# Optimization experiments

Hardware: AMD Instinct MI355X
Metric: run time of the kernel (lower is better)

The kernel has to match this reference:

```python
import jax, jax.numpy as jnp
import numpy as np

NP_, NA, NPR = 3000, 25, 1071
N = NP_ + NA + NPR          # 4096 total nodes
D = 256                     # latent_dim
H = 8                       # num_heads
DH = D // H                 # head dim 32
FF = 4 * D                  # feed-forward dim
BLOCKS = 3                  # args.block_num
E = 131072                  # edges = N * 32 avg degree
EPS = 1e-5


def setup_inputs() -> dict:
    key = jax.random.key(0)
    ks = jax.random.split(key, 16)
    s = 1.0 / np.sqrt(D)
    return {
        "adj_row": jax.random.randint(ks[0], (E,), 0, N, dtype=jnp.int32),
        "adj_col": jax.random.randint(ks[1], (E,), 0, N, dtype=jnp.int32),
        "adj_val": jax.random.uniform(ks[2], (E,), dtype=jnp.float32),
        "pe": jax.random.normal(ks[3], (NP_, D), dtype=jnp.float32) * s,
        "ae": jax.random.normal(ks[4], (NA, D), dtype=jnp.float32) * s,
        "qe": jax.random.normal(ks[5], (NPR, D), dtype=jnp.float32) * s,
        "Wqkv": jax.random.normal(ks[6], (D, 3 * D), dtype=jnp.float32) * s,
        "Wo": jax.random.normal(ks[7], (D, D), dtype=jnp.float32) * s,
        "W1": jax.random.normal(ks[8], (D, FF), dtype=jnp.float32) * s,
        "b1": jnp.zeros((FF,), dtype=jnp.float32),
        "W2": jax.random.normal(ks[9], (FF, D), dtype=jnp.float32) * (1.0 / np.sqrt(FF)),
        "b2": jnp.zeros((D,), dtype=jnp.float32),
        "ln1_g": jnp.ones((D,), dtype=jnp.float32),
        "ln1_b": jnp.zeros((D,), dtype=jnp.float32),
        "ln2_g": jnp.ones((D,), dtype=jnp.float32),
        "ln2_b": jnp.zeros((D,), dtype=jnp.float32),
    }


def _layer_norm(x, g, b):
    m = jnp.mean(x, axis=-1, keepdims=True)
    v = jnp.mean(jnp.square(x - m), axis=-1, keepdims=True)
    return (x - m) * jax.lax.rsqrt(v + EPS) * g + b


def _encoder_layer(x, Wqkv, Wo, W1, b1, W2, b2, ln1_g, ln1_b, ln2_g, ln2_b):
    # x: [N, D]; standard post-LN transformer encoder (dropout = 0)
    qkv = x @ Wqkv                                   # [N, 3D]
    q, k, v = jnp.split(qkv, 3, axis=-1)
    q = q.reshape(N, H, DH)
    k = k.reshape(N, H, DH)
    v = v.reshape(N, H, DH)
    scores = jnp.einsum("nhd,mhd->hnm", q, k) / np.sqrt(DH)  # [H, N, N]
    att = jax.nn.softmax(scores, axis=-1)
    o = jnp.einsum("hnm,mhd->nhd", att, v).reshape(N, D) @ Wo
    x = _layer_norm(x + o, ln1_g, ln1_b)
    h = jax.nn.relu(x @ W1 + b1) @ W2 + b2
    return _layer_norm(x + h, ln2_g, ln2_b)


def _spmm(adj_row, adj_col, adj_val, x):
    # sparse [N,N] @ dense [N,D] via gather + segment-sum scatter
    msgs = adj_val[:, None] * x[adj_col]             # [E, D]
    return jax.ops.segment_sum(msgs, adj_row, num_segments=N)


def reference(adj_row, adj_col, adj_val, pe, ae, qe, Wqkv, Wo, W1, b1, W2, b2,
              ln1_g, ln1_b, ln2_g, ln2_b):
    cur = jnp.concatenate([pe, ae, qe], axis=0)      # [N, D]
    total = cur
    for _ in range(BLOCKS):
        t = _spmm(adj_row, adj_col, adj_val, cur)
        t = _encoder_layer(t, Wqkv, Wo, W1, b1, W2, b2, ln1_g, ln1_b, ln2_g, ln2_b)
        cur = t + cur                                # residual per block
        total = total + cur                          # sum over embeds list
    protein = total[:NP_]
    aa = total[NP_:NP_ + NA]
    prop = total[NP_ + NA:]
    return total, protein, aa, prop
```

## Files before the change

kernel.cpp:

```cpp
#include <hip/hip_runtime.h>
#include <hip/hip_bf16.h>


#define NPROT 3000
#define NAA   25
#define NPROP 1071
#define NTOT  4096
#define DIM   256
#define NH    8
#define DHD   32
#define FFD   1024
#define NEDGE 131072
#define LNEPS 1e-5f
#define KSPLIT 4
#define KVQ (NTOT/KSPLIT)

typedef unsigned short u16;
typedef __attribute__((ext_vector_type(8))) short short8v;
typedef __attribute__((ext_vector_type(4))) float float4v;
typedef __attribute__((ext_vector_type(2))) unsigned int uint2v;

__device__ __forceinline__ u16 f2bu(float x){
  union { __hip_bfloat16 h; u16 u; } c; c.h = __float2bfloat16(x); return c.u;
}
__device__ __forceinline__ float bu2f(u16 u){
  union { unsigned int i; float f; } c; c.i = ((unsigned int)u) << 16; return c.f;
}
__device__ __forceinline__ float4v mfma16(short8v a, short8v b, float4v c){
  return __builtin_amdgcn_mfma_f32_16x16x32_bf16(a, b, c, 0, 0, 0);
}

__global__ __launch_bounds__(256) void k_embed(const float* __restrict__ pe, const float* __restrict__ ae,
                                               const float* __restrict__ qe,
                                               float* __restrict__ cur, float* __restrict__ tot){
  int i = blockIdx.x*256 + threadIdx.x;
  int row = i >> 8;
  float v;
  if (row < NPROT)           v = pe[i];
  else if (row < NPROT+NAA)  v = ae[i - NPROT*DIM];
  else                       v = qe[i - (NPROT+NAA)*DIM];
  cur[i] = v; tot[i] = v;
}

__global__ __launch_bounds__(256) void k_zero(int* __restrict__ p, int n){
  int i = blockIdx.x*256 + threadIdx.x; if (i < n) p[i] = 0;
}

__global__ __launch_bounds__(256) void k_wconv(const float* __restrict__ W, u16* __restrict__ Wt,
                                               int K, int N){
  int n = blockIdx.x;
  for (int k = threadIdx.x; k < K; k += 256)
    Wt[(size_t)n*K + k] = f2bu(W[(size_t)k*N + n]);
}

__global__ __launch_bounds__(256) void k_hist(const int* __restrict__ rows, int* __restrict__ cnt){
  int e = blockIdx.x*256 + threadIdx.x; if (e < NEDGE) atomicAdd(&cnt[rows[e]], 1);
}

__global__ __launch_bounds__(64) void k_scan(const int* __restrict__ cnt, int* __restrict__ rowptr,
                                             int* __restrict__ cursor){
  int lane = threadIdx.x;
  int sum = 0;
  for (int i = 0; i < 64; ++i) sum += cnt[lane*64 + i];
  int pref = sum;
  #pragma unroll
  for (int off = 1; off < 64; off <<= 1){
    int u = __shfl_up(pref, off);
    if (lane >= off) pref += u;
  }
  int run = pref - sum;
  for (int i = 0; i < 64; ++i){
    int c = cnt[lane*64 + i];
    rowptr[lane*64 + i] = run;
    cursor[lane*64 + i] = run;
    run += c;
  }
  if (lane == 63) rowptr[NTOT] = run;
}

__global__ __launch_bounds__(256) void k_scatter(const int* __restrict__ rows, const int* __restrict__ cols,
                                                 const float* __restrict__ vals, int* __restrict__ cursor,
                                                 int* __restrict__ ccol, float* __restrict__ cval){
  int e = blockIdx.x*256 + threadIdx.x; if (e >= NEDGE) return;
  int p = atomicAdd(&cursor[rows[e]], 1);
  ccol[p] = cols[e]; cval[p] = vals[e];
}

__global__ __launch_bounds__(256) void k_spmm(const int* __restrict__ rowptr, const int* __restrict__ ccol,
                                              const float* __restrict__ cval, const float* __restrict__ x,
                                              float* __restrict__ out, u16* __restrict__ outb){
  int r = blockIdx.x, c = threadIdx.x;
  int s = rowptr[r], e = rowptr[r+1];
  float acc = 0.f;
  for (int i = s; i < e; ++i)
    acc += cval[i] * x[((size_t)ccol[i] << 8) + c];
  out[((size_t)r << 8) + c] = acc;
  outb[((size_t)r << 8) + c] = f2bu(acc);
}

template<int RELU, int BIAS, int BF16OUT>
__global__ __launch_bounds__(256) void k_gemm_mfma(const u16* __restrict__ A, const u16* __restrict__ Wt,
                                                   const float* __restrict__ bias, void* __restrict__ Cv,
                                                   int M, int K, int Nc){
  __shared__ u16 Al[128*64];
  __shared__ u16 Bl[128*64];
  const int tid = threadIdx.x;
  const int w  = tid >> 6, l = tid & 63, lr = l & 15, g = l >> 4;
  const int row0 = blockIdx.y*128, col0 = blockIdx.x*128;
  const int wm = (w >> 1)*64, wn = (w & 1)*64;
  const int sm = tid >> 1;
  const int so = (tid & 1)*4;
  float4v acc[4][4] = {};

  for (int k0 = 0; k0 < K; k0 += 64){
    const u16* As = A  + (size_t)(row0 + sm)*K + k0 + so*8;
    const u16* Bs = Wt + (size_t)(col0 + sm)*K + k0 + so*8;
    #pragma unroll
    for (int j = 0; j < 4; ++j){
      int o = so + j;
      int slot = o ^ (sm & 7);
      *(short8v*)(Al + sm*64 + slot*8) = *(const short8v*)(As + j*8);
      *(short8v*)(Bl + sm*64 + slot*8) = *(const short8v*)(Bs + j*8);
    }
    __syncthreads();
    #pragma unroll
    for (int kk = 0; kk < 2; ++kk){
      short8v af[4], bfr[4];
      #pragma unroll
      for (int i = 0; i < 4; ++i){
        int am = wm + 16*i + lr;
        af[i]  = *(const short8v*)(Al + am*64 + (((4*kk + g) ^ (am & 7))*8));
        int bn = wn + 16*i + lr;
        bfr[i] = *(const short8v*)(Bl + bn*64 + (((4*kk + g) ^ (bn & 7))*8));
      }
      #pragma unroll
      for (int mi = 0; mi < 4; ++mi)
        #pragma unroll
        for (int ni = 0; ni < 4; ++ni)
          acc[mi][ni] = mfma16(af[mi], bfr[ni], acc[mi][ni]);
    }
    __syncthreads();
  }

  #pragma unroll
  for (int mi = 0; mi < 4; ++mi){
    #pragma unroll
    for (int ni = 0; ni < 4; ++ni){
      int col = col0 + wn + 16*ni + lr;
      float bv = BIAS ? bias[col] : 0.f;
      #pragma unroll
      for (int j = 0; j < 4; ++j){
        int row = row0 + wm + 16*mi + 4*g + j;
        float v = acc[mi][ni][j] + bv;
        if (RELU) v = fmaxf(v, 0.f);
        if (BF16OUT) ((u16*)Cv)[(size_t)row*Nc + col] = f2bu(v);
        else         ((float*)Cv)[(size_t)row*Nc + col] = v;
      }
    }
  }
}

__global__ __launch_bounds__(256) void k_attn_mfma(const u16* __restrict__ qbf,
                                                   u16* __restrict__ op,
                                                   float* __restrict__ mbuf, float* __restrict__ lbuf){
  __shared__ u16 Vt[2][32*64];
  __shared__ u16 Pl[4][16*64];
  __shared__ float Fl[4][16];
  const int h   = blockIdx.y;
  const int ks  = blockIdx.z;
  const int qb  = blockIdx.x * 64;
  const int tid = threadIdx.x;
  const int w   = tid >> 6;
  const int l   = tid & 63;
  const int lr  = l & 15;
  const int g   = l >> 4;
  const int sr  = tid >> 2;
  const int sq  = tid & 3;
  const float SC  = 0.17677669529663687f;
  const float SCL = 0.25503837f;
  u16* opart = op + (size_t)ks*NTOT*DIM;

  short8v qf = *(const short8v*)(qbf + (size_t)(qb + 16*w + lr)*768 + h*DHD + 8*g);

  float4v oa0 = {0.f,0.f,0.f,0.f}, oa1 = {0.f,0.f,0.f,0.f};
  float mrun = -1e30f, lrun = 0.f;
  u16* pw = &Pl[w][0];

  const u16* vp = qbf + (size_t)(ks*KVQ + sr)*768 + 512 + h*DHD + 8*sq;
  const u16* kp = qbf + (size_t)(ks*KVQ + lr)*768 + 256 + h*DHD + 8*g;
  short8v vreg = *(const short8v*)vp;
  short8v kf0 = *(const short8v*)(kp);
  short8v kf1 = *(const short8v*)(kp + (size_t)16*768);
  short8v kf2 = *(const short8v*)(kp + (size_t)32*768);
  short8v kf3 = *(const short8v*)(kp + (size_t)48*768);

  const int NIT = KVQ/64;
  for (int t = 0; t < NIT; ++t){
    u16* vt = &Vt[t & 1][0];
    #pragma unroll
    for (int j = 0; j < 8; ++j){
      int row  = 8*sq + j;
      int slot = (sr >> 3) ^ j;
      vt[row*64 + slot*8 + (sr & 7)] = (u16)vreg[j];
    }
    __syncthreads();
    vp += (size_t)64*768;
    if (t + 1 < NIT) vreg = *(const short8v*)vp;

    float4v s0 = mfma16(kf0, qf, (float4v){0.f,0.f,0.f,0.f});
    float4v s1 = mfma16(kf1, qf, (float4v){0.f,0.f,0.f,0.f});
    float4v s2 = mfma16(kf2, qf, (float4v){0.f,0.f,0.f,0.f});
    float4v s3 = mfma16(kf3, qf, (float4v){0.f,0.f,0.f,0.f});
    if (t + 1 < NIT){
      const u16* kn = kp + (size_t)(t+1)*64*768;
      kf0 = *(const short8v*)(kn);
      kf1 = *(const short8v*)(kn + (size_t)16*768);
      kf2 = *(const short8v*)(kn + (size_t)32*768);
      kf3 = *(const short8v*)(kn + (size_t)48*768);
    }

    float tm = fmaxf(fmaxf(fmaxf(s0[0],s0[1]),fmaxf(s0[2],s0[3])),
              fmaxf(fmaxf(fmaxf(s1[0],s1[1]),fmaxf(s1[2],s1[3])),
              fmaxf(fmaxf(fmaxf(s2[0],s2[1]),fmaxf(s2[2],s2[3])),
                    fmaxf(fmaxf(s3[0],s3[1]),fmaxf(s3[2],s3[3])))));
    tm = fmaxf(tm, __shfl_xor(tm, 16));
    tm = fmaxf(tm, __shfl_xor(tm, 32));
    float mn  = fmaxf(mrun, tm);
    float fac = exp2f((mrun - mn)*SCL);
    float mns = mn*SCL;
    mrun = mn;
    float rs = 0.f;
    #pragma unroll
    for (int j = 0; j < 4; ++j){
      float p0 = exp2f(__builtin_fmaf(s0[j], SCL, -mns)); s0[j] = p0;
      float p1 = exp2f(__builtin_fmaf(s1[j], SCL, -mns)); s1[j] = p1;
      float p2 = exp2f(__builtin_fmaf(s2[j], SCL, -mns)); s2[j] = p2;
      float p3 = exp2f(__builtin_fmaf(s3[j], SCL, -mns)); s3[j] = p3;
      rs += (p0 + p1) + (p2 + p3);
    }
    rs += __shfl_xor(rs, 16);
    rs += __shfl_xor(rs, 32);
    lrun = lrun*fac + rs;
    if (g == 0) Fl[w][lr] = fac;

    {
      unsigned int a0 = (unsigned)f2bu(s0[0]) | ((unsigned)f2bu(s0[1]) << 16);
      unsigned int b0 = (unsigned)f2bu(s0[2]) | ((unsigned)f2bu(s0[3]) << 16);
      unsigned int a1 = (unsigned)f2bu(s1[0]) | ((unsigned)f2bu(s1[1]) << 16);
      unsigned int b1 = (unsigned)f2bu(s1[2]) | ((unsigned)f2bu(s1[3]) << 16);
      unsigned int a2 = (unsigned)f2bu(s2[0]) | ((unsigned)f2bu(s2[1]) << 16);
      unsigned int b2 = (unsigned)f2bu(s2[2]) | ((unsigned)f2bu(s2[3]) << 16);
      unsigned int a3 = (unsigned)f2bu(s3[0]) | ((unsigned)f2bu(s3[1]) << 16);
      unsigned int b3 = (unsigned)f2bu(s3[2]) | ((unsigned)f2bu(s3[3]) << 16);
      int gh = g >> 1, gl = 4*(g & 1);
      uint2v* d0 = (uint2v*)(pw + lr*64 + ((0 + gh) ^ (lr & 7))*8 + gl);
      uint2v* d1 = (uint2v*)(pw + lr*64 + ((2 + gh) ^ (lr & 7))*8 + gl);
      uint2v* d2 = (uint2v*)(pw + lr*64 + ((4 + gh) ^ (lr & 7))*8 + gl);
      uint2v* d3 = (uint2v*)(pw + lr*64 + ((6 + gh) ^ (lr & 7))*8 + gl);
      *d0 = (uint2v){a0, b0};
      *d1 = (uint2v){a1, b1};
      *d2 = (uint2v){a2, b2};
      *d3 = (uint2v){a3, b3};
    }

    float fq0 = Fl[w][4*g+0], fq1 = Fl[w][4*g+1], fq2 = Fl[w][4*g+2], fq3 = Fl[w][4*g+3];
    oa0[0]*=fq0; oa0[1]*=fq1; oa0[2]*=fq2; oa0[3]*=fq3;
    oa1[0]*=fq0; oa1[1]*=fq1; oa1[2]*=fq2; oa1[3]*=fq3;

    #pragma unroll
    for (int kk = 0; kk < 2; ++kk){
      int slotp = (4*kk + g) ^ (lr & 7);
      short8v pa = *(const short8v*)(pw + lr*64 + slotp*8);
      short8v v0 = *(const short8v*)(vt + lr*64        + slotp*8);
      short8v v1 = *(const short8v*)(vt + (lr+16)*64   + slotp*8);
      oa0 = mfma16(pa, v0, oa0);
      oa1 = mfma16(pa, v1, oa1);
    }
  }

  #pragma unroll
  for (int j = 0; j < 4; ++j){
    size_t row = (size_t)(qb + 16*w + 4*g + j);
    opart[row*DIM + h*DHD + lr]      = f2bu(oa0[j]);
    opart[row*DIM + h*DHD + 16 + lr] = f2bu(oa1[j]);
  }
  if (l < 16){
    size_t mi = (size_t)(ks*NH + h)*NTOT + qb + 16*w + lr;
    mbuf[mi] = mrun*SC;
    lbuf[mi] = lrun;
  }
}

__global__ __launch_bounds__(256) void k_attn_merge(const u16* __restrict__ op,
                                                    const float* __restrict__ mbuf, const float* __restrict__ lbuf,
                                                    u16* __restrict__ obf){
  int i = blockIdx.x*256 + threadIdx.x;
  int r = i >> 8, c = i & 255, h = c >> 5;
  float m[KSPLIT], wgt[KSPLIT];
  float M = -1e30f;
  #pragma unroll
  for (int k = 0; k < KSPLIT; ++k){
    m[k] = mbuf[(size_t)(k*NH + h)*NTOT + r];
    M = fmaxf(M, m[k]);
  }
  float L = 0.f, acc = 0.f;
  #pragma unroll
  for (int k = 0; k < KSPLIT; ++k){
    wgt[k] = __expf(m[k] - M);
    L   += wgt[k]*lbuf[(size_t)(k*NH + h)*NTOT + r];
    acc += wgt[k]*bu2f(op[(size_t)k*NTOT*DIM + i]);
  }
  obf[i] = f2bu(acc / L);
}

template<int DUAL>
__global__ __launch_bounds__(256) void k_add_ln(const float* __restrict__ a, const float* __restrict__ b,
                                                const float* __restrict__ g, const float* __restrict__ be,
                                                float* __restrict__ out, u16* __restrict__ out2){
  __shared__ float red[4];
  int r = blockIdx.x, c = threadIdx.x;
  float v = a[((size_t)r << 8) + c] + b[((size_t)r << 8) + c];
  float s = v;
  #pragma unroll
  for (int off = 32; off; off >>= 1) s += __shfl_down(s, off);
  if ((c & 63) == 0) red[c >> 6] = s;
  __syncthreads();
  float mean = (red[0]+red[1]+red[2]+red[3]) * (1.f/DIM);
  __syncthreads();
  float d = v - mean;
  float s2 = d*d;
  #pragma unroll
  for (int off = 32; off; off >>= 1) s2 += __shfl_down(s2, off);
  if ((c & 63) == 0) red[c >> 6] = s2;
  __syncthreads();
  float var = (red[0]+red[1]+red[2]+red[3]) * (1.f/DIM);
  float rv = d * rsqrtf(var + LNEPS) * g[c] + be[c];
  out[((size_t)r << 8) + c] = rv;
  if (DUAL) out2[((size_t)r << 8) + c] = f2bu(rv);
}

__global__ __launch_bounds__(256) void k_update(const float* __restrict__ x2, float* __restrict__ cur,
                                                float* __restrict__ tot){
  int i = blockIdx.x*256 + threadIdx.x;
  float c = cur[i] + x2[i];
  cur[i] = c;
  tot[i] += c;
}

__global__ __launch_bounds__(256) void k_out(const float* __restrict__ tot, float* __restrict__ out){
  int i = blockIdx.x*256 + threadIdx.x;
  float v = tot[i];
  out[i] = v;
  out[NTOT*DIM + i] = v;
}

extern "C" void kernel_launch(void* const* d_in, const int* in_sizes, int n_in,
                              void* d_out, int out_size, void* d_ws, size_t ws_size,
                              hipStream_t stream){
  const int*   adj_row = (const int*)  d_in[0];
  const int*   adj_col = (const int*)  d_in[1];
  const float* adj_val = (const float*)d_in[2];
  const float* pe   = (const float*)d_in[3];
  const float* ae   = (const float*)d_in[4];
  const float* qe   = (const float*)d_in[5];
  const float* Wqkv = (const float*)d_in[6];
  const float* Wo   = (const float*)d_in[7];
  const float* W1   = (const float*)d_in[8];
  const float* b1   = (const float*)d_in[9];
  const float* W2   = (const float*)d_in[10];
  const float* b2   = (const float*)d_in[11];
  const float* g1   = (const float*)d_in[12];
  const float* be1  = (const float*)d_in[13];
  const float* g2   = (const float*)d_in[14];
  const float* be2  = (const float*)d_in[15];
  float* out = (float*)d_out;

  char* w = (char*)d_ws;
  float* cur  = (float*)w; w += (size_t)NTOT*DIM*4;
  float* tot  = (float*)w; w += (size_t)NTOT*DIM*4;
  float* tf   = (float*)w; w += (size_t)NTOT*DIM*4;
  float* pbuf = (float*)w; w += (size_t)NTOT*DIM*4;
  float* x1   = (float*)w; w += (size_t)NTOT*DIM*4;
  u16* tbf    = (u16*)w;   w += (size_t)NTOT*DIM*2;
  u16* obf    = (u16*)w;   w += (size_t)NTOT*DIM*2;
  u16* x1b    = (u16*)w;   w += (size_t)NTOT*DIM*2;
  u16* hq     = (u16*)w;   w += (size_t)NTOT*FFD*2;
  u16* wqkvt  = (u16*)w;   w += (size_t)768*256*2;
  u16* wot    = (u16*)w;   w += (size_t)256*256*2;
  u16* w1t    = (u16*)w;   w += (size_t)1024*256*2;
  u16* w2t    = (u16*)w;   w += (size_t)256*1024*2;
  int* rowptr = (int*)w;   w += (size_t)(NTOT+1)*4;
  int* cnt    = (int*)w;   w += (size_t)NTOT*4;
  int* cursor = (int*)w;   w += (size_t)NTOT*4;
  int* ccol   = (int*)w;   w += (size_t)NEDGE*4;
  float* cval = (float*)w; w += (size_t)NEDGE*4;
  u16* qbf  = hq;
  u16* opbf = (u16*)pbuf;
  float* mbuf = (float*)tbf;
  float* lbuf = mbuf + (size_t)KSPLIT*NH*NTOT;

  k_zero<<<16, 256, 0, stream>>>(cnt, NTOT);
  k_embed<<<NTOT, 256, 0, stream>>>(pe, ae, qe, cur, tot);
  k_hist<<<NEDGE/256, 256, 0, stream>>>(adj_row, cnt);
  k_scan<<<1, 64, 0, stream>>>(cnt, rowptr, cursor);
  k_scatter<<<NEDGE/256, 256, 0, stream>>>(adj_row, adj_col, adj_val, cursor, ccol, cval);
  k_wconv<<<768,  256, 0, stream>>>(Wqkv, wqkvt, 256, 768);
  k_wconv<<<256,  256, 0, stream>>>(Wo,   wot,   256, 256);
  k_wconv<<<1024, 256, 0, stream>>>(W1,   w1t,   256, 1024);
  k_wconv<<<256,  256, 0, stream>>>(W2,   w2t,  1024, 256);

  for (int blk = 0; blk < 3; ++blk){
    k_spmm<<<NTOT, 256, 0, stream>>>(rowptr, ccol, cval, cur, tf, tbf);
    k_gemm_mfma<0,0,1><<<dim3(768/128, NTOT/128), 256, 0, stream>>>(tbf, wqkvt, nullptr, qbf, NTOT, 256, 768);
    k_attn_mfma<<<dim3(NTOT/64, NH, KSPLIT), 256, 0, stream>>>(qbf, opbf, mbuf, lbuf);
    k_attn_merge<<<NTOT*DIM/256, 256, 0, stream>>>(opbf, mbuf, lbuf, obf);
    k_gemm_mfma<0,0,0><<<dim3(256/128, NTOT/128), 256, 0, stream>>>(obf, wot, nullptr, pbuf, NTOT, 256, 256);
    k_add_ln<1><<<NTOT, 256, 0, stream>>>(tf, pbuf, g1, be1, x1, x1b);
    k_gemm_mfma<1,1,1><<<dim3(1024/128, NTOT/128), 256, 0, stream>>>(x1b, w1t, b1, hq, NTOT, 256, 1024);
    k_gemm_mfma<0,1,0><<<dim3(256/128, NTOT/128), 256, 0, stream>>>(hq, w2t, b2, pbuf, NTOT, 1024, 256);
    k_add_ln<0><<<NTOT, 256, 0, stream>>>(x1, pbuf, g2, be2, tf, nullptr);
    k_update<<<NTOT, 256, 0, stream>>>(tf, cur, tot);
  }
  k_out<<<NTOT, 256, 0, stream>>>(tot, out);
}
```

Before: 566.6 us.

## Shrink GEMM tiles to 64x64, skip redundant softmax rescale, fuse LN with update

Replaces the 128x128 MFMA GEMM with a 64x64-tile variant so each small GEMM launches more workgroups and fills more compute units. In attention, the online-softmax rescale of the output accumulator and the LDS factor exchange are skipped when no lane in the wavefront sees a new row maximum. The second add+LayerNorm is fused with the residual and total update, which removes one kernel launch and one round trip of the activation through memory. Smaller tiles lower data reuse per workgroup, and the wave-uniform branch adds a vote on every attention iteration.

```diff
diff --git a/kernel.cpp b/kernel.cpp
--- a/kernel.cpp
+++ b/kernel.cpp
@@ -99,24 +99,24 @@
 }
 
 template<int RELU, int BIAS, int BF16OUT>
-__global__ __launch_bounds__(256) void k_gemm_mfma(const u16* __restrict__ A, const u16* __restrict__ Wt,
-                                                   const float* __restrict__ bias, void* __restrict__ Cv,
-                                                   int M, int K, int Nc){
-  __shared__ u16 Al[128*64];
-  __shared__ u16 Bl[128*64];
+__global__ __launch_bounds__(256) void k_gemm64(const u16* __restrict__ A, const u16* __restrict__ Wt,
+                                                const float* __restrict__ bias, void* __restrict__ Cv,
+                                                int M, int K, int Nc){
+  __shared__ u16 Al[64*64];
+  __shared__ u16 Bl[64*64];
   const int tid = threadIdx.x;
   const int w  = tid >> 6, l = tid & 63, lr = l & 15, g = l >> 4;
-  const int row0 = blockIdx.y*128, col0 = blockIdx.x*128;
-  const int wm = (w >> 1)*64, wn = (w & 1)*64;
-  const int sm = tid >> 1;
-  const int so = (tid & 1)*4;
-  float4v acc[4][4] = {};
+  const int row0 = blockIdx.y*64, col0 = blockIdx.x*64;
+  const int wm = (w >> 1)*32, wn = (w & 1)*32;
+  const int sm = tid >> 2;
+  const int so = (tid & 3)*2;
+  float4v acc[2][2] = {};
 
   for (int k0 = 0; k0 < K; k0 += 64){
     const u16* As = A  + (size_t)(row0 + sm)*K + k0 + so*8;
     const u16* Bs = Wt + (size_t)(col0 + sm)*K + k0 + so*8;
     #pragma unroll
-    for (int j = 0; j < 4; ++j){
+    for (int j = 0; j < 2; ++j){
       int o = so + j;
       int slot = o ^ (sm & 7);
       *(short8v*)(Al + sm*64 + slot*8) = *(const short8v*)(As + j*8);
@@ -125,27 +125,26 @@
     __syncthreads();
     #pragma unroll
     for (int kk = 0; kk < 2; ++kk){
-      short8v af[4], bfr[4];
+      short8v af[2], bfr[2];
       #pragma unroll
-      for (int i = 0; i < 4; ++i){
+      for (int i = 0; i < 2; ++i){
         int am = wm + 16*i + lr;
         af[i]  = *(const short8v*)(Al + am*64 + (((4*kk + g) ^ (am & 7))*8));
         int bn = wn + 16*i + lr;
         bfr[i] = *(const short8v*)(Bl + bn*64 + (((4*kk + g) ^ (bn & 7))*8));
       }
-      #pragma unroll
-      for (int mi = 0; mi < 4; ++mi)
-        #pragma unroll
-        for (int ni = 0; ni < 4; ++ni)
-          acc[mi][ni] = mfma16(af[mi], bfr[ni], acc[mi][ni]);
+      acc[0][0] = mfma16(af[0], bfr[0], acc[0][0]);
+      acc[0][1] = mfma16(af[0], bfr[1], acc[0][1]);
+      acc[1][0] = mfma16(af[1], bfr[0], acc[1][0]);
+      acc[1][1] = mfma16(af[1], bfr[1], acc[1][1]);
     }
     __syncthreads();
   }
 
   #pragma unroll
-  for (int mi = 0; mi < 4; ++mi){
-    #pragma unroll
-    for (int ni = 0; ni < 4; ++ni){
+  for (int mi = 0; mi < 2; ++mi){
+    #pragma unroll
+    for (int ni = 0; ni < 2; ++ni){
       int col = col0 + wn + 16*ni + lr;
       float bv = BIAS ? bias[col] : 0.f;
       #pragma unroll
@@ -225,10 +224,14 @@
                     fmaxf(fmaxf(s3[0],s3[1]),fmaxf(s3[2],s3[3])))));
     tm = fmaxf(tm, __shfl_xor(tm, 16));
     tm = fmaxf(tm, __shfl_xor(tm, 32));
-    float mn  = fmaxf(mrun, tm);
-    float fac = exp2f((mrun - mn)*SCL);
-    float mns = mn*SCL;
-    mrun = mn;
+    const bool nomax = __all(tm <= mrun);
+    float fac = 1.f;
+    if (!nomax){
+      float mn = fmaxf(mrun, tm);
+      fac = exp2f((mrun - mn)*SCL);
+      mrun = mn;
+    }
+    float mns = mrun*SCL;
     float rs = 0.f;
     #pragma unroll
     for (int j = 0; j < 4; ++j){
@@ -240,8 +243,6 @@
     }
     rs += __shfl_xor(rs, 16);
     rs += __shfl_xor(rs, 32);
-    lrun = lrun*fac + rs;
-    if (g == 0) Fl[w][lr] = fac;
 
     {
       unsigned int a0 = (unsigned)f2bu(s0[0]) | ((unsigned)f2bu(s0[1]) << 16);
@@ -263,9 +264,15 @@
       *d3 = (uint2v){a3, b3};
     }
 
-    float fq0 = Fl[w][4*g+0], fq1 = Fl[w][4*g+1], fq2 = Fl[w][4*g+2], fq3 = Fl[w][4*g+3];
-    oa0[0]*=fq0; oa0[1]*=fq1; oa0[2]*=fq2; oa0[3]*=fq3;
-    oa1[0]*=fq0; oa1[1]*=fq1; oa1[2]*=fq2; oa1[3]*=fq3;
+    if (!nomax){
+      lrun = lrun*fac + rs;
+      if (g == 0) Fl[w][lr] = fac;
+      float fq0 = Fl[w][4*g+0], fq1 = Fl[w][4*g+1], fq2 = Fl[w][4*g+2], fq3 = Fl[w][4*g+3];
+      oa0[0]*=fq0; oa0[1]*=fq1; oa0[2]*=fq2; oa0[3]*=fq3;
+      oa1[0]*=fq0; oa1[1]*=fq1; oa1[2]*=fq2; oa1[3]*=fq3;
+    } else {
+      lrun += rs;
+    }
 
     #pragma unroll
     for (int kk = 0; kk < 2; ++kk){
@@ -339,12 +346,31 @@
   if (DUAL) out2[((size_t)r << 8) + c] = f2bu(rv);
 }
 
-__global__ __launch_bounds__(256) void k_update(const float* __restrict__ x2, float* __restrict__ cur,
-                                                float* __restrict__ tot){
-  int i = blockIdx.x*256 + threadIdx.x;
-  float c = cur[i] + x2[i];
-  cur[i] = c;
-  tot[i] += c;
+__global__ __launch_bounds__(256) void k_add_ln_upd(const float* __restrict__ a, const float* __restrict__ b,
+                                                    const float* __restrict__ g, const float* __restrict__ be,
+                                                    float* __restrict__ cur, float* __restrict__ tot){
+  __shared__ float red[4];
+  int r = blockIdx.x, c = threadIdx.x;
+  size_t idx = ((size_t)r << 8) + c;
+  float v = a[idx] + b[idx];
+  float s = v;
+  #pragma unroll
+  for (int off = 32; off; off >>= 1) s += __shfl_down(s, off);
+  if ((c & 63) == 0) red[c >> 6] = s;
+  __syncthreads();
+  float mean = (red[0]+red[1]+red[2]+red[3]) * (1.f/DIM);
+  __syncthreads();
+  float d = v - mean;
+  float s2 = d*d;
+  #pragma unroll
+  for (int off = 32; off; off >>= 1) s2 += __shfl_down(s2, off);
+  if ((c & 63) == 0) red[c >> 6] = s2;
+  __syncthreads();
+  float var = (red[0]+red[1]+red[2]+red[3]) * (1.f/DIM);
+  float rv = d * rsqrtf(var + LNEPS) * g[c] + be[c];
+  float cu = cur[idx] + rv;
+  cur[idx] = cu;
+  tot[idx] += cu;
 }
 
 __global__ __launch_bounds__(256) void k_out(const float* __restrict__ tot, float* __restrict__ out){
@@ -411,15 +437,14 @@
 
   for (int blk = 0; blk < 3; ++blk){
     k_spmm<<<NTOT, 256, 0, stream>>>(rowptr, ccol, cval, cur, tf, tbf);
-    k_gemm_mfma<0,0,1><<<dim3(768/128, NTOT/128), 256, 0, stream>>>(tbf, wqkvt, nullptr, qbf, NTOT, 256, 768);
+    k_gemm64<0,0,1><<<dim3(768/64, NTOT/64), 256, 0, stream>>>(tbf, wqkvt, nullptr, qbf, NTOT, 256, 768);
     k_attn_mfma<<<dim3(NTOT/64, NH, KSPLIT), 256, 0, stream>>>(qbf, opbf, mbuf, lbuf);
     k_attn_merge<<<NTOT*DIM/256, 256, 0, stream>>>(opbf, mbuf, lbuf, obf);
-    k_gemm_mfma<0,0,0><<<dim3(256/128, NTOT/128), 256, 0, stream>>>(obf, wot, nullptr, pbuf, NTOT, 256, 256);
+    k_gemm64<0,0,0><<<dim3(256/64, NTOT/64), 256, 0, stream>>>(obf, wot, nullptr, pbuf, NTOT, 256, 256);
     k_add_ln<1><<<NTOT, 256, 0, stream>>>(tf, pbuf, g1, be1, x1, x1b);
-    k_gemm_mfma<1,1,1><<<dim3(1024/128, NTOT/128), 256, 0, stream>>>(x1b, w1t, b1, hq, NTOT, 256, 1024);
-    k_gemm_mfma<0,1,0><<<dim3(256/128, NTOT/128), 256, 0, stream>>>(hq, w2t, b2, pbuf, NTOT, 1024, 256);
-    k_add_ln<0><<<NTOT, 256, 0, stream>>>(x1, pbuf, g2, be2, tf, nullptr);
-    k_update<<<NTOT, 256, 0, stream>>>(tf, cur, tot);
+    k_gemm64<1,1,1><<<dim3(1024/64, NTOT/64), 256, 0, stream>>>(x1b, w1t, b1, hq, NTOT, 256, 1024);
+    k_gemm64<0,1,0><<<dim3(256/64, NTOT/64), 256, 0, stream>>>(hq, w2t, b2, pbuf, NTOT, 1024, 256);
+    k_add_ln_upd<<<NTOT, 256, 0, stream>>>(x1, pbuf, g2, be2, cur, tot);
   }
   k_out<<<NTOT, 256, 0, stream>>>(tot, out);
 }
```

Result: faster. 497.3 us (-12.2%).
